# Kernel optimization log

Hardware: AMD Instinct MI355X
Metric: run time of the kernel (lower is better)

Reference implementation:

```python
import jax, jax.numpy as jnp
import numpy as np

VOCAB = 50257
EMBED = 512
HEADS = 8
HEAD_DIM = EMBED // HEADS
WINDOW = 128
NUM_CLASS = 20
B, S = 4, 2048


def setup_inputs() -> dict:
    key = jax.random.key(0)
    ks = jax.random.split(key, 16)
    sc = 0.02
    inp = {
        'text': jax.random.randint(ks[0], (B, S), 0, VOCAB),
        'emb': jax.random.normal(ks[1], (VOCAB, EMBED), jnp.float32) * sc,
        'in_w': jax.random.normal(ks[2], (3 * EMBED, EMBED), jnp.float32) * sc,
        'in_b': jnp.zeros((3 * EMBED,), jnp.float32),
        'out_w': jax.random.normal(ks[3], (EMBED, EMBED), jnp.float32) * sc,
        'out_b': jnp.zeros((EMBED,), jnp.float32),
        'w1': jax.random.normal(ks[4], (512, EMBED), jnp.float32) * sc,
        'b1': jnp.zeros((512,), jnp.float32),
        'w2': jax.random.normal(ks[5], (256, 512), jnp.float32) * sc,
        'b2': jnp.zeros((256,), jnp.float32),
        'w3': jax.random.normal(ks[6], (128, 256), jnp.float32) * sc,
        'b3': jnp.zeros((128,), jnp.float32),
        'w4': jax.random.normal(ks[7], (NUM_CLASS, 128), jnp.float32) * sc,
        'b4': jnp.zeros((NUM_CLASS,), jnp.float32),
    }
    return inp


def _banded_mask(seq_len, window):
    i = jnp.arange(seq_len)[:, None]
    j = jnp.arange(seq_len)[None, :]
    allowed = jnp.abs(i - j) <= window  # band of width 2*window+1
    return jnp.where(allowed, 0.0, -jnp.inf).astype(jnp.float32)


def reference(text, emb, in_w, in_b, out_w, out_b, w1, b1, w2, b2, w3, b3, w4, b4):
    # Embedding lookup (dropout is identity in eval mode)
    x = emb[text]  # [B, S, E]
    b, s, e = x.shape

    # torch nn.MultiheadAttention: packed in_proj, scaling by 1/sqrt(head_dim)
    wq, wk, wv = in_w[:e], in_w[e:2 * e], in_w[2 * e:]
    bq, bk, bv = in_b[:e], in_b[e:2 * e], in_b[2 * e:]
    q = (x @ wq.T + bq).reshape(b, s, HEADS, HEAD_DIM)
    k = (x @ wk.T + bk).reshape(b, s, HEADS, HEAD_DIM)
    v = (x @ wv.T + bv).reshape(b, s, HEADS, HEAD_DIM)

    mask = _banded_mask(s, WINDOW)  # [S, S] additive, -inf outside band
    scores = jnp.einsum('bihd,bjhd->bhij', q, k) / jnp.sqrt(jnp.float32(HEAD_DIM))
    probs = jax.nn.softmax(scores + mask, axis=-1)  # [B, H, S, S]
    attn = jnp.einsum('bhij,bjhd->bihd', probs, v).reshape(b, s, e)
    attn = attn @ out_w.T + out_b  # [B, S, E]

    # max-pool over sequence
    ctx = jnp.max(attn, axis=1)  # [B, E]

    # MLP head with leaky_relu (negative_slope=0.01, torch default)
    h = jax.nn.leaky_relu(ctx @ w1.T + b1, 0.01)
    h = jax.nn.leaky_relu(h @ w2.T + b2, 0.01)
    h = jax.nn.leaky_relu(h @ w3.T + b3, 0.01)
    return h @ w4.T + b4  # [B, NUM_CLASS]
```

## Files before the change

### kernel.cpp

```cpp
#include <hip/hip_runtime.h>

typedef unsigned short u16;
typedef __attribute__((ext_vector_type(8))) short bf16x8;
typedef __attribute__((ext_vector_type(4))) float f32x4;

#define S_LEN 2048
#define EMBED 512
#define HEADS 8
#define HDIM 64
#define BATCH 4
#define TOKENS (BATCH * S_LEN)

__device__ __forceinline__ u16 f2bf(float f) {
  union { float f; unsigned u; } v;
  v.f = f;
  unsigned r = v.u + 0x7fffu + ((v.u >> 16) & 1u);
  return (u16)(r >> 16);
}

__device__ __forceinline__ unsigned fkey(float f) {
  unsigned u = __float_as_uint(f);
  return (u & 0x80000000u) ? ~u : (u | 0x80000000u);
}
__device__ __forceinline__ float funkey(unsigned k) {
  unsigned u = (k & 0x80000000u) ? (k ^ 0x80000000u) : ~k;
  return __uint_as_float(u);
}

__device__ __forceinline__ void gl2lds16(const void* g, void* l) {
  __builtin_amdgcn_global_load_lds(
      (const __attribute__((address_space(1))) void*)g,
      (__attribute__((address_space(3))) void*)l, 16, 0, 0);
}

__global__ __launch_bounds__(256) void prep_kernel(
    const int* __restrict__ text, const float* __restrict__ emb,
    const float* __restrict__ in_w, const float* __restrict__ out_w,
    u16* __restrict__ Xb, u16* __restrict__ Wq, u16* __restrict__ Wo,
    unsigned* __restrict__ ctxi) {
  const int bid = blockIdx.x;
  const int tid = threadIdx.x;
  if (bid < 4096) {
    const int t = bid * 2 + (tid >> 7);
    const int c = (tid & 127) * 4;
    const size_t src = (size_t)text[t] * EMBED + c;
    const float4 v = *(const float4*)(emb + src);
    u16* dst = Xb + (size_t)t * EMBED + c;
    dst[0] = f2bf(v.x); dst[1] = f2bf(v.y); dst[2] = f2bf(v.z); dst[3] = f2bf(v.w);
  } else if (bid < 5120) {
    const int idx4 = ((bid - 4096) * 256 + tid) * 4;
    const float* src;
    u16* dst;
    if (idx4 < 1536 * 512) { src = in_w + idx4; dst = Wq + idx4; }
    else { src = out_w + (idx4 - 1536 * 512); dst = Wo + (idx4 - 1536 * 512); }
    const float4 v = *(const float4*)src;
    dst[0] = f2bf(v.x); dst[1] = f2bf(v.y); dst[2] = f2bf(v.z); dst[3] = f2bf(v.w);
  } else {
    for (int i = tid; i < BATCH * EMBED; i += 256) ctxi[i] = 0u;
  }
}

__global__ __launch_bounds__(256, 3) void qkv_mfma(
    const u16* __restrict__ Xb, const u16* __restrict__ Wq,
    const float* __restrict__ in_b,
    u16* __restrict__ qg, u16* __restrict__ kg, u16* __restrict__ vt) {
  __shared__ u16 SM[16384];
  u16* const As = SM;
  u16* const Bs = SM + 8192;
  const int lid = blockIdx.x;
  const int xcd = lid & 7, idx = lid >> 3;
  const int m0 = (xcd * 8 + idx / 12) * 128;
  const int n0 = (idx % 12) * 128;
  const int tid = threadIdx.x;
  const int w = tid >> 6, l = tid & 63, quad = l >> 4, ln = l & 15;
  const int rb = (w >> 1) * 64, cb = (w & 1) * 64;

  f32x4 acc[4][4] = {};

  for (int k0 = 0; k0 < EMBED; k0 += 64) {
#pragma unroll
    for (int it = 0; it < 4; ++it) {
      const int chunk = it * 256 + tid;
      const int row = chunk >> 3, cp = chunk & 7, c = cp ^ (row & 7);
      gl2lds16(Xb + (size_t)(m0 + row) * EMBED + k0 + c * 8, &As[chunk * 8]);
      gl2lds16(Wq + (size_t)(n0 + row) * EMBED + k0 + c * 8, &Bs[chunk * 8]);
    }
    __syncthreads();
#pragma unroll
    for (int s = 0; s < 2; ++s) {
      bf16x8 af[4], bf[4];
#pragma unroll
      for (int i = 0; i < 4; ++i) {
        const int r = rb + 16 * i + ln;
        af[i] = *(const bf16x8*)&As[r * 64 + (((s << 2) + quad) ^ (r & 7)) * 8];
      }
#pragma unroll
      for (int j = 0; j < 4; ++j) {
        const int n = cb + 16 * j + ln;
        bf[j] = *(const bf16x8*)&Bs[n * 64 + (((s << 2) + quad) ^ (n & 7)) * 8];
      }
#pragma unroll
      for (int i = 0; i < 4; ++i)
#pragma unroll
        for (int j = 0; j < 4; ++j)
          acc[i][j] = __builtin_amdgcn_mfma_f32_16x16x32_bf16(af[i], bf[j], acc[i][j], 0, 0, 0);
    }
    __syncthreads();
  }

  const int b = m0 >> 11;
  if (n0 < 1024) {
#pragma unroll
    for (int j = 0; j < 4; ++j) {
      const int n = n0 + cb + 16 * j + ln;
      const float bias = in_b[n];
      const int sec = n >> 9, f = n & 511, h = f >> 6, d = f & 63;
#pragma unroll
      for (int i = 0; i < 4; ++i) {
#pragma unroll
        for (int r = 0; r < 4; ++r) {
          const int t = m0 + rb + 16 * i + quad * 4 + r;
          const int s = t & 2047;
          const float val = acc[i][j][r] + bias;
          if (sec == 0)
            qg[((size_t)((b * HEADS + h) * S_LEN + s)) * HDIM + d] = f2bf(val * 0.125f);
          else
            kg[((size_t)((b * HEADS + h) * S_LEN + s)) * HDIM + d] = f2bf(val);
        }
      }
    }
  } else {
#pragma unroll
    for (int j = 0; j < 4; ++j) {
      const int col = cb + 16 * j + ln;
      const float bias = in_b[n0 + col];
#pragma unroll
      for (int i = 0; i < 4; ++i) {
#pragma unroll
        for (int r = 0; r < 4; ++r) {
          const int row = rb + 16 * i + quad * 4 + r;
          SM[row * 128 + (col ^ (((row >> 3) & 3) << 4))] = f2bf(acc[i][j][r] + bias);
        }
      }
    }
    __syncthreads();
#pragma unroll
    for (int itd = 0; itd < 2; ++itd) {
      const int dl = w * 32 + itd * 16 + ln;
      const int f = (n0 + dl) & 511, h = f >> 6, d = f & 63;
      u16* dst = vt + ((size_t)((b * HEADS + h) * HDIM + d)) * S_LEN + (m0 & 2047);
#pragma unroll
      for (int it2 = 0; it2 < 4; ++it2) {
        const int sb = quad * 8 + it2 * 32;
        const int swc = dl ^ (((sb >> 3) & 3) << 4);
        union { u16 a[8]; bf16x8 v; } u;
#pragma unroll
        for (int k = 0; k < 8; ++k) u.a[k] = SM[(sb + k) * 128 + swc];
        *(bf16x8*)(dst + sb) = u.v;
      }
    }
  }
}

__global__ __launch_bounds__(256, 3) void attn_mfma(
    const u16* __restrict__ qg, const u16* __restrict__ kg,
    const u16* __restrict__ vt, u16* __restrict__ attnb) {
  __shared__ u16 KV[320 * 64];
  __shared__ u16 Pb[4][16 * 40];
  const int lid = blockIdx.x;
  const int nid = (lid & 7) * 128 + (lid >> 3);
  const int bh = nid >> 5;
  const int i0 = (nid & 31) * 64;
  const int jb = i0 - 128;
  const int tid = threadIdx.x;
  const int w = tid >> 6, l = tid & 63, quad = l >> 4, ln = l & 15;
  const int jlo = w, jhi = w + 16;

  const u16* qrow = qg + ((size_t)bh * S_LEN + i0 + w * 16 + ln) * HDIM;
  bf16x8 qf[2];
  qf[0] = *(const bf16x8*)(qrow + quad * 8);
  qf[1] = *(const bf16x8*)(qrow + 32 + quad * 8);

  const u16* kbase = kg + (size_t)bh * S_LEN * HDIM;
#pragma unroll
  for (int it = 0; it < 10; ++it) {
    const int chunk = it * 256 + tid;
    const int row = chunk >> 3, cp = chunk & 7, c = cp ^ (row & 7);
    int gj = jb + row;
    gj = gj < 0 ? 0 : (gj > S_LEN - 1 ? S_LEN - 1 : gj);
    gl2lds16(kbase + (size_t)gj * HDIM + c * 8, &KV[chunk * 8]);
  }
  __syncthreads();

  f32x4 sc[20] = {};
#pragma unroll
  for (int jt = 0; jt < 20; ++jt) {
    if (jt < jlo || jt > jhi) continue;
    const int r = jt * 16 + ln;
    const bf16x8 b0 = *(const bf16x8*)&KV[r * 64 + ((quad) ^ (r & 7)) * 8];
    const bf16x8 b1 = *(const bf16x8*)&KV[r * 64 + ((4 + quad) ^ (r & 7)) * 8];
    f32x4 a = {};
    a = __builtin_amdgcn_mfma_f32_16x16x32_bf16(qf[0], b0, a, 0, 0, 0);
    a = __builtin_amdgcn_mfma_f32_16x16x32_bf16(qf[1], b1, a, 0, 0, 0);
    sc[jt] = a;
  }
  __syncthreads();

  const u16* vbase = vt + (size_t)bh * HDIM * S_LEN;
#pragma unroll
  for (int it = 0; it < 10; ++it) {
    const int chunk = it * 256 + tid;
    const int row = chunk / 40, cp = chunk % 40, c = cp ^ (row & 7);
    int gc = jb + c * 8;
    gc = gc < 0 ? 0 : (gc > S_LEN - 8 ? S_LEN - 8 : gc);
    gl2lds16(vbase + (size_t)row * S_LEN + gc, &KV[chunk * 8]);
  }

  const int gibase = i0 + w * 16 + quad * 4;
  int lo[4], hi[4];
#pragma unroll
  for (int r = 0; r < 4; ++r) {
    const int gi = gibase + r;
    int lr = gi - 128, hr = gi + 128;
    lo[r] = lr < 0 ? 0 : lr;
    hi[r] = hr > S_LEN - 1 ? S_LEN - 1 : hr;
  }
  float mrow[4] = {-1e30f, -1e30f, -1e30f, -1e30f}, lrow[4];
#pragma unroll
  for (int jt = 0; jt < 20; ++jt) {
    if (jt < jlo || jt > jhi) continue;
    const int gj = jb + jt * 16 + ln;
#pragma unroll
    for (int r = 0; r < 4; ++r) {
      const bool valid = (gj >= lo[r]) && (gj <= hi[r]);
      const float v = valid ? sc[jt][r] : -1e30f;
      sc[jt][r] = v;
      mrow[r] = fmaxf(mrow[r], v);
    }
  }
#pragma unroll
  for (int r = 0; r < 4; ++r) {
    mrow[r] = fmaxf(mrow[r], __shfl_xor(mrow[r], 1));
    mrow[r] = fmaxf(mrow[r], __shfl_xor(mrow[r], 2));
    mrow[r] = fmaxf(mrow[r], __shfl_xor(mrow[r], 4));
    mrow[r] = fmaxf(mrow[r], __shfl_xor(mrow[r], 8));
    lrow[r] = 0.f;
  }
#pragma unroll
  for (int jt = 0; jt < 20; ++jt) {
    if (jt < jlo || jt > jhi) continue;
#pragma unroll
    for (int r = 0; r < 4; ++r) {
      const float e = __expf(sc[jt][r] - mrow[r]);
      sc[jt][r] = e;
      lrow[r] += e;
    }
  }
#pragma unroll
  for (int r = 0; r < 4; ++r) {
    lrow[r] += __shfl_xor(lrow[r], 1);
    lrow[r] += __shfl_xor(lrow[r], 2);
    lrow[r] += __shfl_xor(lrow[r], 4);
    lrow[r] += __shfl_xor(lrow[r], 8);
    lrow[r] = 1.0f / lrow[r];
  }

  __syncthreads();

  f32x4 oacc[4] = {};
  u16* pb = &Pb[w][0];
#pragma unroll
  for (int kt = 0; kt < 10; ++kt) {
    if (kt * 2 + 1 < jlo || kt * 2 > jhi) continue;
#pragma unroll
    for (int tt = 0; tt < 2; ++tt) {
      const int jt = kt * 2 + tt;
#pragma unroll
      for (int r = 0; r < 4; ++r)
        pb[(quad * 4 + r) * 40 + ln + 16 * tt] = f2bf(sc[jt][r]);
    }
    __asm__ volatile("" ::: "memory");
    const bf16x8 pa = *(const bf16x8*)&pb[ln * 40 + quad * 8];
#pragma unroll
    for (int dt = 0; dt < 4; ++dt) {
      const int d = dt * 16 + ln;
      const bf16x8 vb = *(const bf16x8*)&KV[d * 320 + ((kt * 4 + quad) ^ (d & 7)) * 8];
      oacc[dt] = __builtin_amdgcn_mfma_f32_16x16x32_bf16(pa, vb, oacc[dt], 0, 0, 0);
    }
  }

  const int b = bh >> 3, h = bh & 7;
#pragma unroll
  for (int dt = 0; dt < 4; ++dt) {
    const int d = h * HDIM + dt * 16 + ln;
#pragma unroll
    for (int r = 0; r < 4; ++r) {
      const int gi = i0 + w * 16 + quad * 4 + r;
      attnb[((size_t)(b * S_LEN + gi)) * EMBED + d] = f2bf(oacc[dt][r] * lrow[r]);
    }
  }
}

__global__ __launch_bounds__(256, 3) void outproj_mfma(
    const u16* __restrict__ attnb, const u16* __restrict__ Wo,
    const float* __restrict__ out_b, unsigned* __restrict__ ctxi) {
  __shared__ u16 As[128 * 64];
  __shared__ u16 Bs[64 * 64];
  __shared__ float red[4][32];
  const int lid = blockIdx.x;
  const int xcd = lid & 7, idx = lid >> 3;
  const int m0 = (xcd * 8 + (idx >> 3)) * 128;
  const int n0 = (idx & 7) * 64;
  const int tid = threadIdx.x;
  const int w = tid >> 6, l = tid & 63, quad = l >> 4, ln = l & 15;
  const int rb = (w >> 1) * 64, cb = (w & 1) * 32;

  f32x4 acc[4][2] = {};

  for (int k0 = 0; k0 < EMBED; k0 += 64) {
#pragma unroll
    for (int it = 0; it < 4; ++it) {
      const int chunk = it * 256 + tid;
      const int row = chunk >> 3, cp = chunk & 7, c = cp ^ (row & 7);
      gl2lds16(attnb + (size_t)(m0 + row) * EMBED + k0 + c * 8, &As[chunk * 8]);
    }
#pragma unroll
    for (int it = 0; it < 2; ++it) {
      const int chunk = it * 256 + tid;
      const int row = chunk >> 3, cp = chunk & 7, c = cp ^ (row & 7);
      gl2lds16(Wo + (size_t)(n0 + row) * EMBED + k0 + c * 8, &Bs[chunk * 8]);
    }
    __syncthreads();
#pragma unroll
    for (int s = 0; s < 2; ++s) {
      bf16x8 af[4], bf[2];
#pragma unroll
      for (int i = 0; i < 4; ++i) {
        const int r = rb + 16 * i + ln;
        af[i] = *(const bf16x8*)&As[r * 64 + (((s << 2) + quad) ^ (r & 7)) * 8];
      }
#pragma unroll
      for (int j = 0; j < 2; ++j) {
        const int n = cb + 16 * j + ln;
        bf[j] = *(const bf16x8*)&Bs[n * 64 + (((s << 2) + quad) ^ (n & 7)) * 8];
      }
#pragma unroll
      for (int i = 0; i < 4; ++i)
#pragma unroll
        for (int j = 0; j < 2; ++j)
          acc[i][j] = __builtin_amdgcn_mfma_f32_16x16x32_bf16(af[i], bf[j], acc[i][j], 0, 0, 0);
    }
    __syncthreads();
  }

  float cm[2];
#pragma unroll
  for (int j = 0; j < 2; ++j) {
    float m = -1e30f;
#pragma unroll
    for (int i = 0; i < 4; ++i)
#pragma unroll
      for (int r = 0; r < 4; ++r) m = fmaxf(m, acc[i][j][r]);
    m = fmaxf(m, __shfl_xor(m, 16));
    m = fmaxf(m, __shfl_xor(m, 32));
    cm[j] = m;
  }
  if (l < 16) {
#pragma unroll
    for (int j = 0; j < 2; ++j) red[w][16 * j + ln] = cm[j];
  }
  __syncthreads();
  if (tid < 64) {
    const int half = tid >> 5;
    const int cc = tid & 31;
    const float m = fmaxf(red[half][cc], red[half + 2][cc]);
    const int n = n0 + tid;
    const int b = m0 >> 11;
    atomicMax(&ctxi[b * EMBED + n], fkey(m + out_b[n]));
  }
}

__global__ __launch_bounds__(256) void mlp_l1(
    const unsigned* __restrict__ ctxi, const float* __restrict__ w1,
    const float* __restrict__ b1, float* __restrict__ h1g) {
  __shared__ float ctx[512];
  const int b = blockIdx.x >> 5, chunk = blockIdx.x & 31;
  const int tid = threadIdx.x;
  for (int e = tid; e < 512; e += 256) ctx[e] = funkey(ctxi[b * 512 + e]);
  __syncthreads();

  const int og = tid >> 4, ln = tid & 15;
  const int o = chunk * 16 + og;
  const float4* wv = (const float4*)(w1 + (size_t)o * 512 + ln * 32);
  const float4* xv = (const float4*)(ctx + ln * 32);
  float acc = 0.f;
#pragma unroll
  for (int k = 0; k < 8; ++k) {
    const float4 a = wv[k], x = xv[k];
    acc += a.x * x.x + a.y * x.y + a.z * x.z + a.w * x.w;
  }
  acc += __shfl_xor(acc, 1);
  acc += __shfl_xor(acc, 2);
  acc += __shfl_xor(acc, 4);
  acc += __shfl_xor(acc, 8);
  if (ln == 0) {
    const float a = acc + b1[o];
    h1g[b * 512 + o] = a > 0.f ? a : 0.01f * a;
  }
}

__global__ __launch_bounds__(256) void mlp_l2(
    const float* __restrict__ h1g, const float* __restrict__ w2,
    const float* __restrict__ b2, float* __restrict__ h2g) {
  __shared__ float xb[512];
  const int b = blockIdx.x >> 4, chunk = blockIdx.x & 15;
  const int tid = threadIdx.x;
  for (int e = tid; e < 512; e += 256) xb[e] = h1g[b * 512 + e];
  __syncthreads();

  const int og = tid >> 4, ln = tid & 15;
  const int o = chunk * 16 + og;
  const float4* wv = (const float4*)(w2 + (size_t)o * 512 + ln * 32);
  const float4* xv = (const float4*)(xb + ln * 32);
  float acc = 0.f;
#pragma unroll
  for (int k = 0; k < 8; ++k) {
    const float4 a = wv[k], x = xv[k];
    acc += a.x * x.x + a.y * x.y + a.z * x.z + a.w * x.w;
  }
  acc += __shfl_xor(acc, 1);
  acc += __shfl_xor(acc, 2);
  acc += __shfl_xor(acc, 4);
  acc += __shfl_xor(acc, 8);
  if (ln == 0) {
    const float a = acc + b2[o];
    h2g[b * 256 + o] = a > 0.f ? a : 0.01f * a;
  }
}

__global__ __launch_bounds__(256) void mlp_l34(
    const float* __restrict__ h2g,
    const float* __restrict__ w3, const float* __restrict__ b3,
    const float* __restrict__ w4, const float* __restrict__ b4,
    float* __restrict__ out) {
  __shared__ float xb[256], h3[128];
  const int b = blockIdx.x, tid = threadIdx.x;
  if (tid < 256) xb[tid] = h2g[b * 256 + tid];
  __syncthreads();

  {
    const int o = tid >> 1, kh = tid & 1;
    float acc = 0.f;
    const float* wr = w3 + (size_t)o * 256 + kh * 128;
    const float* xr = xb + kh * 128;
    for (int k = 0; k < 128; k += 4) {
      const float4 wv = *(const float4*)(wr + k);
      const float4 xv = *(const float4*)(xr + k);
      acc += wv.x * xv.x + wv.y * xv.y + wv.z * xv.z + wv.w * xv.w;
    }
    acc += __shfl_xor(acc, 1);
    if (kh == 0) { const float a = acc + b3[o]; h3[o] = a > 0.f ? a : 0.01f * a; }
  }
  __syncthreads();

  if (tid < 160) {
    const int o = tid >> 3, ks = tid & 7;
    const float* wr = w4 + (size_t)o * 128 + ks * 16;
    const float* xr = h3 + ks * 16;
    float acc = 0.f;
    for (int k = 0; k < 16; k += 4) {
      const float4 wv = *(const float4*)(wr + k);
      const float4 xv = *(const float4*)(xr + k);
      acc += wv.x * xv.x + wv.y * xv.y + wv.z * xv.z + wv.w * xv.w;
    }
    acc += __shfl_xor(acc, 1);
    acc += __shfl_xor(acc, 2);
    acc += __shfl_xor(acc, 4);
    if (ks == 0) out[b * 20 + o] = acc + b4[o];
  }
}

extern "C" void kernel_launch(void* const* d_in, const int* in_sizes, int n_in,
                              void* d_out, int out_size, void* d_ws, size_t ws_size,
                              hipStream_t stream) {
  (void)in_sizes; (void)n_in; (void)out_size; (void)ws_size;
  const int*   text  = (const int*)d_in[0];
  const float* emb   = (const float*)d_in[1];
  const float* in_w  = (const float*)d_in[2];
  const float* in_b  = (const float*)d_in[3];
  const float* out_w = (const float*)d_in[4];
  const float* out_b = (const float*)d_in[5];
  const float* w1 = (const float*)d_in[6];
  const float* b1 = (const float*)d_in[7];
  const float* w2 = (const float*)d_in[8];
  const float* b2 = (const float*)d_in[9];
  const float* w3 = (const float*)d_in[10];
  const float* b3 = (const float*)d_in[11];
  const float* w4 = (const float*)d_in[12];
  const float* b4 = (const float*)d_in[13];

  char* ws = (char*)d_ws;
  u16* Xb   = (u16*)(ws);
  u16* Wq   = (u16*)(ws + 8388608);
  u16* Wo   = (u16*)(ws + 9961472);
  u16* qg   = (u16*)(ws + 10485760);
  u16* kg   = (u16*)(ws + 18874368);
  u16* vt   = (u16*)(ws + 27262976);
  u16* attn = (u16*)(ws + 35651584);
  unsigned* ctxi = (unsigned*)(ws + 44040192);
  float* h1g  = (float*)(ws + 44048384);
  float* h2g  = (float*)(ws + 44056576);

  prep_kernel<<<5121, 256, 0, stream>>>(text, emb, in_w, out_w, Xb, Wq, Wo, ctxi);
  qkv_mfma<<<768, 256, 0, stream>>>(Xb, Wq, in_b, qg, kg, vt);
  attn_mfma<<<1024, 256, 0, stream>>>(qg, kg, vt, attn);
  outproj_mfma<<<512, 256, 0, stream>>>(attn, Wo, out_b, ctxi);
  mlp_l1<<<128, 256, 0, stream>>>(ctxi, w1, b1, h1g);
  mlp_l2<<<64, 256, 0, stream>>>(h1g, w2, b2, h2g);
  mlp_l34<<<4, 256, 0, stream>>>(h2g, w3, b3, w4, b4, (float*)d_out);
}
```

Measured before the change: 222.0 us.

## Enlarge attention query block to 128 rows and specialize interior band masking

The attention kernel now handles 128 query rows per block with 8 waves and a 384-key shared K/V window, where it previously used 64 rows and a 320-key window. This cuts redundant K/V staging per query and halves the block count. It also adds a fast path for interior blocks that masks only the first and last diagonal tiles instead of bounds-checking every score. The costs are more LDS per block and some extra boundary-tile MFMA work, since each wave now always computes 17 tiles.

```diff
diff --git a/kernel.cpp b/kernel.cpp
--- a/kernel.cpp
+++ b/kernel.cpp
@@ -162,19 +162,20 @@
   }
 }
 
-__global__ __launch_bounds__(256, 3) void attn_mfma(
+#define QBLK 128
+#define WND 384
+__global__ __launch_bounds__(512, 4) void attn_mfma(
     const u16* __restrict__ qg, const u16* __restrict__ kg,
     const u16* __restrict__ vt, u16* __restrict__ attnb) {
-  __shared__ u16 KV[320 * 64];
-  __shared__ u16 Pb[4][16 * 40];
+  __shared__ u16 KV[WND * 64];
+  __shared__ u16 Pb[8][16 * 40];
   const int lid = blockIdx.x;
-  const int nid = (lid & 7) * 128 + (lid >> 3);
-  const int bh = nid >> 5;
-  const int i0 = (nid & 31) * 64;
+  const int nid = (lid & 7) * 64 + (lid >> 3);
+  const int bh = nid >> 4;
+  const int i0 = (nid & 15) * QBLK;
   const int jb = i0 - 128;
   const int tid = threadIdx.x;
   const int w = tid >> 6, l = tid & 63, quad = l >> 4, ln = l & 15;
-  const int jlo = w, jhi = w + 16;
 
   const u16* qrow = qg + ((size_t)bh * S_LEN + i0 + w * 16 + ln) * HDIM;
   bf16x8 qf[2];
@@ -183,8 +184,8 @@
 
   const u16* kbase = kg + (size_t)bh * S_LEN * HDIM;
 #pragma unroll
-  for (int it = 0; it < 10; ++it) {
-    const int chunk = it * 256 + tid;
+  for (int it = 0; it < 6; ++it) {
+    const int chunk = it * 512 + tid;
     const int row = chunk >> 3, cp = chunk & 7, c = cp ^ (row & 7);
     int gj = jb + row;
     gj = gj < 0 ? 0 : (gj > S_LEN - 1 ? S_LEN - 1 : gj);
@@ -192,50 +193,68 @@
   }
   __syncthreads();
 
-  f32x4 sc[20] = {};
-#pragma unroll
-  for (int jt = 0; jt < 20; ++jt) {
-    if (jt < jlo || jt > jhi) continue;
-    const int r = jt * 16 + ln;
+  f32x4 sc[18] = {};
+#pragma unroll
+  for (int jj = 0; jj < 17; ++jj) {
+    const int r = (w + jj) * 16 + ln;
     const bf16x8 b0 = *(const bf16x8*)&KV[r * 64 + ((quad) ^ (r & 7)) * 8];
     const bf16x8 b1 = *(const bf16x8*)&KV[r * 64 + ((4 + quad) ^ (r & 7)) * 8];
     f32x4 a = {};
     a = __builtin_amdgcn_mfma_f32_16x16x32_bf16(qf[0], b0, a, 0, 0, 0);
     a = __builtin_amdgcn_mfma_f32_16x16x32_bf16(qf[1], b1, a, 0, 0, 0);
-    sc[jt] = a;
+    sc[jj] = a;
   }
   __syncthreads();
 
   const u16* vbase = vt + (size_t)bh * HDIM * S_LEN;
 #pragma unroll
-  for (int it = 0; it < 10; ++it) {
-    const int chunk = it * 256 + tid;
-    const int row = chunk / 40, cp = chunk % 40, c = cp ^ (row & 7);
+  for (int it = 0; it < 6; ++it) {
+    const int chunk = it * 512 + tid;
+    const int row = chunk / 48, cp = chunk % 48, c = cp ^ (row & 7);
     int gc = jb + c * 8;
     gc = gc < 0 ? 0 : (gc > S_LEN - 8 ? S_LEN - 8 : gc);
     gl2lds16(vbase + (size_t)row * S_LEN + gc, &KV[chunk * 8]);
   }
 
-  const int gibase = i0 + w * 16 + quad * 4;
-  int lo[4], hi[4];
-#pragma unroll
-  for (int r = 0; r < 4; ++r) {
-    const int gi = gibase + r;
-    int lr = gi - 128, hr = gi + 128;
-    lo[r] = lr < 0 ? 0 : lr;
-    hi[r] = hr > S_LEN - 1 ? S_LEN - 1 : hr;
-  }
+  const bool interior = (jb >= 0) && (jb + WND <= S_LEN);
   float mrow[4] = {-1e30f, -1e30f, -1e30f, -1e30f}, lrow[4];
-#pragma unroll
-  for (int jt = 0; jt < 20; ++jt) {
-    if (jt < jlo || jt > jhi) continue;
-    const int gj = jb + jt * 16 + ln;
+  const int q4 = quad * 4;
+  if (interior) {
 #pragma unroll
     for (int r = 0; r < 4; ++r) {
-      const bool valid = (gj >= lo[r]) && (gj <= hi[r]);
-      const float v = valid ? sc[jt][r] : -1e30f;
-      sc[jt][r] = v;
-      mrow[r] = fmaxf(mrow[r], v);
+      {
+        const float v = (q4 + r <= ln) ? sc[0][r] : -1e30f;
+        sc[0][r] = v; mrow[r] = fmaxf(mrow[r], v);
+      }
+      {
+        const float v = (q4 + r >= ln) ? sc[16][r] : -1e30f;
+        sc[16][r] = v; mrow[r] = fmaxf(mrow[r], v);
+      }
+    }
+#pragma unroll
+    for (int jj = 1; jj < 16; ++jj)
+#pragma unroll
+      for (int r = 0; r < 4; ++r) mrow[r] = fmaxf(mrow[r], sc[jj][r]);
+  } else {
+    const int gibase = i0 + w * 16 + q4;
+    int lo[4], hi[4];
+#pragma unroll
+    for (int r = 0; r < 4; ++r) {
+      const int gi = gibase + r;
+      int lr = gi - 128, hr = gi + 128;
+      lo[r] = lr < 0 ? 0 : lr;
+      hi[r] = hr > S_LEN - 1 ? S_LEN - 1 : hr;
+    }
+#pragma unroll
+    for (int jj = 0; jj < 17; ++jj) {
+      const int gj = jb + (w + jj) * 16 + ln;
+#pragma unroll
+      for (int r = 0; r < 4; ++r) {
+        const bool valid = (gj >= lo[r]) && (gj <= hi[r]);
+        const float v = valid ? sc[jj][r] : -1e30f;
+        sc[jj][r] = v;
+        mrow[r] = fmaxf(mrow[r], v);
+      }
     }
   }
 #pragma unroll
@@ -247,15 +266,13 @@
     lrow[r] = 0.f;
   }
 #pragma unroll
-  for (int jt = 0; jt < 20; ++jt) {
-    if (jt < jlo || jt > jhi) continue;
+  for (int jj = 0; jj < 17; ++jj)
 #pragma unroll
     for (int r = 0; r < 4; ++r) {
-      const float e = __expf(sc[jt][r] - mrow[r]);
-      sc[jt][r] = e;
+      const float e = __expf(sc[jj][r] - mrow[r]);
+      sc[jj][r] = e;
       lrow[r] += e;
     }
-  }
 #pragma unroll
   for (int r = 0; r < 4; ++r) {
     lrow[r] += __shfl_xor(lrow[r], 1);
@@ -270,21 +287,22 @@
   f32x4 oacc[4] = {};
   u16* pb = &Pb[w][0];
 #pragma unroll
-  for (int kt = 0; kt < 10; ++kt) {
-    if (kt * 2 + 1 < jlo || kt * 2 > jhi) continue;
+  for (int kt = 0; kt < 9; ++kt) {
 #pragma unroll
     for (int tt = 0; tt < 2; ++tt) {
-      const int jt = kt * 2 + tt;
+      const int s = kt * 2 + tt;
 #pragma unroll
       for (int r = 0; r < 4; ++r)
-        pb[(quad * 4 + r) * 40 + ln + 16 * tt] = f2bf(sc[jt][r]);
+        pb[(q4 + r) * 40 + ln + 16 * tt] = f2bf(sc[s][r]);
     }
     __asm__ volatile("" ::: "memory");
     const bf16x8 pa = *(const bf16x8*)&pb[ln * 40 + quad * 8];
 #pragma unroll
     for (int dt = 0; dt < 4; ++dt) {
       const int d = dt * 16 + ln;
-      const bf16x8 vb = *(const bf16x8*)&KV[d * 320 + ((kt * 4 + quad) ^ (d & 7)) * 8];
+      int cc = 2 * w + kt * 4 + quad;
+      cc = cc > 47 ? 47 : cc;
+      const bf16x8 vb = *(const bf16x8*)&KV[d * WND + (cc ^ (d & 7)) * 8];
       oacc[dt] = __builtin_amdgcn_mfma_f32_16x16x32_bf16(pa, vb, oacc[dt], 0, 0, 0);
     }
   }
@@ -295,7 +313,7 @@
     const int d = h * HDIM + dt * 16 + ln;
 #pragma unroll
     for (int r = 0; r < 4; ++r) {
-      const int gi = i0 + w * 16 + quad * 4 + r;
+      const int gi = i0 + w * 16 + q4 + r;
       attnb[((size_t)(b * S_LEN + gi)) * EMBED + d] = f2bf(oacc[dt][r] * lrow[r]);
     }
   }
@@ -513,7 +531,7 @@
 
   prep_kernel<<<5121, 256, 0, stream>>>(text, emb, in_w, out_w, Xb, Wq, Wo, ctxi);
   qkv_mfma<<<768, 256, 0, stream>>>(Xb, Wq, in_b, qg, kg, vt);
-  attn_mfma<<<1024, 256, 0, stream>>>(qg, kg, vt, attn);
+  attn_mfma<<<512, 512, 0, stream>>>(qg, kg, vt, attn);
   outproj_mfma<<<512, 256, 0, stream>>>(attn, Wo, out_b, ctxi);
   mlp_l1<<<128, 256, 0, stream>>>(ctxi, w1, b1, h1g);
   mlp_l2<<<64, 256, 0, stream>>>(h1g, w2, b2, h2g);
```

After: 232.7 us. 4.8% more time.
